# Kernel optimization log

Hardware: AMD Instinct MI355X
Metric: run time of the kernel (lower is better)

Reference implementation:

```python
import jax, jax.numpy as jnp
import numpy as np

D_MODEL = 1024
H = 16
D_K = D_MODEL // H
D_FF = 4096
EPS = 1e-6
NEG = -1e9


def setup_inputs() -> dict:
    key = jax.random.key(0)
    ks = jax.random.split(key, 8)
    B, S = 2, 2048
    src = jax.random.normal(ks[0], (B, S, D_MODEL), dtype=jnp.float32)
    src_mask = jnp.ones((B, 1, 1, S), dtype=jnp.int32)
    sc = 1.0 / np.sqrt(D_MODEL)
    wq = jax.random.normal(ks[1], (D_MODEL, D_MODEL), jnp.float32) * sc
    wk = jax.random.normal(ks[2], (D_MODEL, D_MODEL), jnp.float32) * sc
    wv = jax.random.normal(ks[3], (D_MODEL, D_MODEL), jnp.float32) * sc
    wo = jax.random.normal(ks[4], (D_MODEL, D_MODEL), jnp.float32) * sc
    w1 = jax.random.normal(ks[5], (D_FF, D_MODEL), jnp.float32) * sc
    b1 = jnp.zeros((D_FF,), jnp.float32)
    w2 = jax.random.normal(ks[6], (D_MODEL, D_FF), jnp.float32) * (1.0 / np.sqrt(D_FF))
    b2 = jnp.zeros((D_MODEL,), jnp.float32)
    a1 = jnp.ones((1,), jnp.float32)
    be1 = jnp.zeros((1,), jnp.float32)
    a2 = jnp.ones((1,), jnp.float32)
    be2 = jnp.zeros((1,), jnp.float32)
    return dict(src=src, src_mask=src_mask, wq=wq, wk=wk, wv=wv, wo=wo,
                w1=w1, b1=b1, w2=w2, b2=b2, a1=a1, be1=be1, a2=a2, be2=be2)


def layer_norm(x, alpha, bias):
    # torch: mean + unbiased std (ddof=1), eps added to std
    mean = jnp.mean(x, axis=-1, keepdims=True)
    std = jnp.sqrt(jnp.var(x, axis=-1, keepdims=True, ddof=1))
    return alpha * (x - mean) / (std + EPS) + bias


def mha(x, mask, wq, wk, wv, wo):
    B, S, _ = x.shape
    def split(t):  # [B,S,D] -> [B,H,S,D_K]
        return t.reshape(B, S, H, D_K).transpose(0, 2, 1, 3)
    q = split(x @ wq.T)
    k = split(x @ wk.T)
    v = split(x @ wv.T)
    scores = jnp.einsum('bhqd,bhkd->bhqk', q, k) / np.sqrt(D_K)
    scores = jnp.where(mask == 0, NEG, scores)
    attn = jax.nn.softmax(scores, axis=-1)
    out = jnp.einsum('bhqk,bhkd->bhqd', attn, v)
    out = out.transpose(0, 2, 1, 3).reshape(B, S, D_MODEL)
    return out @ wo.T


def reference(src, src_mask, wq, wk, wv, wo, w1, b1, w2, b2, a1, be1, a2, be2):
    x = layer_norm(src, a1, be1)
    src = src + mha(x, src_mask, wq, wk, wv, wo)
    x = layer_norm(src, a2, be2)
    ff = jax.nn.relu(x @ w1.T + b1) @ w2.T + b2
    return src + ff
```

## Files before the change

### kernel.cpp

```cpp
#include <hip/hip_runtime.h>
#include <hip/hip_bf16.h>

typedef unsigned short u16;
typedef unsigned int u32;
typedef float floatx4 __attribute__((ext_vector_type(4)));
typedef __bf16 bf16x8 __attribute__((ext_vector_type(8)));
typedef u16 ushort4v __attribute__((ext_vector_type(4)));
typedef u16 ushort8v __attribute__((ext_vector_type(8)));

#define DEVI static __device__ __forceinline__

DEVI u16 f2bf(float f) {
    u32 u = __builtin_bit_cast(u32, f);
    u += 0x7fffu + ((u >> 16) & 1u);
    return (u16)(u >> 16);
}
DEVI float bf2f(u16 h) { return __builtin_bit_cast(float, (u32)h << 16); }

DEVI float fexp2(float x) { return __builtin_amdgcn_exp2f(x); }

DEVI void async_cp16(const u16* g, u16* l) {
    __builtin_amdgcn_global_load_lds((const __attribute__((address_space(1))) u32*)g,
                                     (__attribute__((address_space(3))) u32*)l, 16, 0, 0);
}

template<int BM, int BN, int RW, int CW, bool QKV3, int NSPLIT, bool XSWZ,
         bool BIAS, bool RELU, bool RESID, bool OBF16>
__global__ __launch_bounds__(256) void gemm_nt(
    const u16* __restrict__ A,
    const u16* __restrict__ W0, const u16* __restrict__ W1, const u16* __restrict__ W2,
    const float* __restrict__ bias, const float* __restrict__ resid,
    void* __restrict__ o0, void* __restrict__ o1, void* __restrict__ o2,
    void* __restrict__ o3, int K, int lda, int Nper, int NX)
{
    static_assert(RW * CW == 4, "4 waves");
    constexpr int WM = BM / RW, WN = BN / CW;
    constexpr int MI = WM / 16, NI = WN / 16;
    __shared__ __align__(16) u16 As[2][BM * 32];
    __shared__ __align__(16) u16 Bs[2][BN * 32];
    const int tid = threadIdx.x;
    const int w = tid >> 6, lane = tid & 63;
    const int q = lane >> 4, ml = lane & 15;
    const int wr = w / CW, wc = w % CW;
    int bx = blockIdx.x, by = blockIdx.y;
    if (XSWZ) {
        const int gx = gridDim.x, gy = gridDim.y;
        int L = by * gx + bx;
        int xcd = L & 7, s = L >> 3;
        int mb = gy >> 3;
        by = xcd * mb + s % mb;
        bx = s / mb;
    }
    const int m0 = by * BM;
    size_t kbase = 0;
    const u16* W = W0;
    void* outp = o0;
    if (NSPLIT > 1) {
        int part = bx / NX; bx -= part * NX; kbase = (size_t)part * K;
        outp = (part == 0) ? o0 : (part == 1 ? o1 : (part == 2 ? o2 : o3));
    }
    int n0 = bx * BN;
    if (QKV3) {
        int sel = n0 / Nper;
        n0 -= sel * Nper;
        W = (sel == 0) ? W0 : (sel == 1 ? W1 : W2);
        outp = (sel == 0) ? o0 : (sel == 1 ? o1 : o2);
    }

    auto stage = [&](int buf, int kt) {
#pragma unroll
        for (int p = 0; p < BM / 64; ++p) {
            int g = p * 256 + tid;
            int r = g >> 2, s = g & 3;
            int c = s ^ ((r >> 1) & 3);
            async_cp16(A + (size_t)(m0 + r) * lda + kbase + kt + c * 8,
                       &As[buf][(p * 256 + w * 64) * 8]);
        }
#pragma unroll
        for (int p = 0; p < BN / 64; ++p) {
            int g = p * 256 + tid;
            int r = g >> 2, s = g & 3;
            int c = s ^ ((r >> 1) & 3);
            async_cp16(W + (size_t)(n0 + r) * lda + kbase + kt + c * 8,
                       &Bs[buf][(p * 256 + w * 64) * 8]);
        }
    };

    const floatx4 fzero = {0.f, 0.f, 0.f, 0.f};
    floatx4 acc[MI][NI];
#pragma unroll
    for (int i = 0; i < MI; ++i)
#pragma unroll
        for (int j = 0; j < NI; ++j) acc[i][j] = fzero;

    stage(0, 0);
    for (int it = 0, kt = 0; kt < K; ++it, kt += 32) {
        __syncthreads();
        if (kt + 32 < K) stage((it + 1) & 1, kt + 32);
        const u16* Asb = As[it & 1];
        const u16* Bsb = Bs[it & 1];
        bf16x8 af[MI], bfr[NI];
#pragma unroll
        for (int i = 0; i < MI; ++i) {
            int rm = wr * WM + i * 16 + ml;
            int s = q ^ ((rm >> 1) & 3);
            af[i] = *(const bf16x8*)&Asb[(rm * 4 + s) * 8];
        }
#pragma unroll
        for (int j = 0; j < NI; ++j) {
            int rn = wc * WN + j * 16 + ml;
            int s = q ^ ((rn >> 1) & 3);
            bfr[j] = *(const bf16x8*)&Bsb[(rn * 4 + s) * 8];
        }
#pragma unroll
        for (int i = 0; i < MI; ++i)
#pragma unroll
            for (int j = 0; j < NI; ++j)
                acc[i][j] = __builtin_amdgcn_mfma_f32_16x16x32_bf16(af[i], bfr[j], acc[i][j], 0, 0, 0);
    }

#pragma unroll
    for (int j = 0; j < NI; ++j) {
        int gn = n0 + wc * WN + j * 16 + ml;
        float bj = 0.f;
        if (BIAS) bj = bias[gn];
#pragma unroll
        for (int i = 0; i < MI; ++i) {
            int gm0 = m0 + wr * WM + i * 16 + q * 4;
#pragma unroll
            for (int r = 0; r < 4; ++r) {
                size_t idx = (size_t)(gm0 + r) * Nper + gn;
                float v = acc[i][j][r] + bj;
                if (RELU) v = fmaxf(v, 0.f);
                if (RESID) v += resid[idx];
                if (OBF16) ((u16*)outp)[idx] = f2bf(v);
                else       ((float*)outp)[idx] = v;
            }
        }
    }
}

__global__ __launch_bounds__(256, 4) void flash8(
    const u16* __restrict__ Q, const u16* __restrict__ Kg,
    const u16* __restrict__ Vt, const float* __restrict__ biasv,
    u16* __restrict__ O)
{
    __shared__ __align__(16) u16 Ks[2][2][32 * 64];
    __shared__ __align__(16) u16 Vs[2][2][64 * 32];
    const int tid = threadIdx.x;
    const int w = tid >> 6, lane = tid & 63;
    const int qw = w & 1, kv = w >> 1;
    const int q = lane >> 4, ml = lane & 15;
    const int b = blockIdx.y >> 4, h = blockIdx.y & 15;
    const size_t rowQ = (size_t)(b * 2048 + blockIdx.x * 64);
    const float KSC = 0.125f * 1.4426950408889634f;
    const floatx4 fzero = {0.f, 0.f, 0.f, 0.f};

    bf16x8 qa[2][2];
#pragma unroll
    for (int qg = 0; qg < 2; ++qg)
#pragma unroll
        for (int c = 0; c < 2; ++c)
            qa[qg][c] = *(const bf16x8*)&Q[(rowQ + qw * 32 + qg * 16 + ml) * 1024
                                           + h * 64 + q * 8 + c * 32];

    auto stage = [&](int buf, int it) {
        {
            int row = tid >> 3, sl = tid & 7;
            int ch = sl ^ ((row & 3) | (((row >> 3) & 1) << 2));
#pragma unroll
            for (int hf = 0; hf < 2; ++hf) {
                int s0 = hf * 1024 + it * 32;
                async_cp16(Kg + (size_t)(b * 2048 + s0 + row) * 1024 + h * 64 + ch * 8,
                           &Ks[hf][buf][(w * 64) * 8]);
            }
        }
        {
            int row = tid >> 2, sl = tid & 3;
            int ch = sl ^ ((row >> 1) & 3);
#pragma unroll
            for (int hf = 0; hf < 2; ++hf) {
                int s0 = hf * 1024 + it * 32;
                async_cp16(Vt + (size_t)(b * 1024 + h * 64 + row) * 2048 + s0 + ch * 8,
                           &Vs[hf][buf][(w * 64) * 8]);
            }
        }
    };

    floatx4 oacc[2][4];
    float lsum[2] = {0.f, 0.f};
#pragma unroll
    for (int qg = 0; qg < 2; ++qg)
#pragma unroll
        for (int d = 0; d < 4; ++d) oacc[qg][d] = fzero;

    const int swk = (ml & 3) | (((ml >> 2) & 1) << 2);
    const int re = ((ml >> 2) << 3) + (ml & 3);

    stage(0, 0);
    for (int it = 0; it < 32; ++it) {
        __syncthreads();
        if (it + 1 < 32) stage((it + 1) & 1, it + 1);
        const u16* Kb = Ks[kv][it & 1];
        const u16* Vb = Vs[kv][it & 1];
        const int s0 = kv * 1024 + it * 32;

        bf16x8 ke0 = *(const bf16x8*)&Kb[(re + 0) * 64 + ((0 + q) ^ swk) * 8];
        bf16x8 ke1 = *(const bf16x8*)&Kb[(re + 0) * 64 + ((4 + q) ^ swk) * 8];
        bf16x8 ko0 = *(const bf16x8*)&Kb[(re + 4) * 64 + ((0 + q) ^ swk) * 8];
        bf16x8 ko1 = *(const bf16x8*)&Kb[(re + 4) * 64 + ((4 + q) ^ swk) * 8];
        const float4 be = *(const float4*)&biasv[b * 2048 + s0 + q * 8];
        const float4 bo = *(const float4*)&biasv[b * 2048 + s0 + q * 8 + 4];
        bf16x8 pfrag[2];
#pragma unroll
        for (int qg = 0; qg < 2; ++qg) {
            floatx4 te = fzero, to = fzero;
            te = __builtin_amdgcn_mfma_f32_16x16x32_bf16(ke0, qa[qg][0], te, 0, 0, 0);
            te = __builtin_amdgcn_mfma_f32_16x16x32_bf16(ke1, qa[qg][1], te, 0, 0, 0);
            to = __builtin_amdgcn_mfma_f32_16x16x32_bf16(ko0, qa[qg][0], to, 0, 0, 0);
            to = __builtin_amdgcn_mfma_f32_16x16x32_bf16(ko1, qa[qg][1], to, 0, 0, 0);
            float pe0 = fexp2(fmaf(te[0], KSC, be.x));
            float pe1 = fexp2(fmaf(te[1], KSC, be.y));
            float pe2 = fexp2(fmaf(te[2], KSC, be.z));
            float pe3 = fexp2(fmaf(te[3], KSC, be.w));
            float po0 = fexp2(fmaf(to[0], KSC, bo.x));
            float po1 = fexp2(fmaf(to[1], KSC, bo.y));
            float po2 = fexp2(fmaf(to[2], KSC, bo.z));
            float po3 = fexp2(fmaf(to[3], KSC, bo.w));
            lsum[qg] += ((pe0 + pe1) + (pe2 + pe3)) + ((po0 + po1) + (po2 + po3));
            u32 pk[4];
            pk[0] = ((__builtin_bit_cast(u32, pe0) + 0x8000u) >> 16)
                  | ((__builtin_bit_cast(u32, pe1) + 0x8000u) & 0xffff0000u);
            pk[1] = ((__builtin_bit_cast(u32, pe2) + 0x8000u) >> 16)
                  | ((__builtin_bit_cast(u32, pe3) + 0x8000u) & 0xffff0000u);
            pk[2] = ((__builtin_bit_cast(u32, po0) + 0x8000u) >> 16)
                  | ((__builtin_bit_cast(u32, po1) + 0x8000u) & 0xffff0000u);
            pk[3] = ((__builtin_bit_cast(u32, po2) + 0x8000u) >> 16)
                  | ((__builtin_bit_cast(u32, po3) + 0x8000u) & 0xffff0000u);
            pfrag[qg] = __builtin_bit_cast(bf16x8, *(uint4*)pk);
        }
#pragma unroll
        for (int dt = 0; dt < 4; ++dt) {
            int vrow = dt * 16 + ml;
            bf16x8 vf = *(const bf16x8*)&Vb[vrow * 32 + ((q ^ ((vrow >> 1) & 3)) * 8)];
#pragma unroll
            for (int qg = 0; qg < 2; ++qg)
                oacc[qg][dt] = __builtin_amdgcn_mfma_f32_16x16x32_bf16(
                    vf, pfrag[qg], oacc[qg][dt], 0, 0, 0);
        }
    }

    __syncthreads();
    float* sO = (float*)&Ks[0][0][0];
    float* sL = (float*)&Vs[0][0][0];
    if (kv == 1) {
#pragma unroll
        for (int qg = 0; qg < 2; ++qg) {
            sL[(qw * 2 + qg) * 64 + lane] = lsum[qg];
#pragma unroll
            for (int dt = 0; dt < 4; ++dt)
                *(floatx4*)&sO[((qw * 2 + qg) * 4 + dt) * 256 + lane * 4] = oacc[qg][dt];
        }
    }
    __syncthreads();
    if (kv == 1) return;
#pragma unroll
    for (int qg = 0; qg < 2; ++qg) {
        lsum[qg] += sL[(qw * 2 + qg) * 64 + lane];
#pragma unroll
        for (int dt = 0; dt < 4; ++dt)
            oacc[qg][dt] += *(const floatx4*)&sO[((qw * 2 + qg) * 4 + dt) * 256 + lane * 4];
        float ls = lsum[qg];
        ls += __shfl_xor(ls, 16, 64);
        ls += __shfl_xor(ls, 32, 64);
        const float rcp = 1.f / ls;
        const size_t row = rowQ + qw * 32 + qg * 16 + ml;
#pragma unroll
        for (int dt = 0; dt < 4; ++dt)
#pragma unroll
            for (int rp = 0; rp < 4; rp += 2) {
                u32 pk = (u32)f2bf(oacc[qg][dt][rp] * rcp)
                       | ((u32)f2bf(oacc[qg][dt][rp + 1] * rcp) << 16);
                *(u32*)&O[row * 1024 + h * 64 + dt * 16 + q * 4 + rp] = pk;
            }
    }
}

__global__ __launch_bounds__(256) void vtrans(const u16* __restrict__ Vb, u16* __restrict__ Vt)
{
    __shared__ __align__(16) u16 T[64 * 72];
    const int tid = threadIdx.x;
    const int ct = blockIdx.x, rt = blockIdx.y;
    const int b = rt >> 5;
    const int s0 = (rt & 31) * 64;
    const int c0 = ct * 64;
#pragma unroll
    for (int p = 0; p < 2; ++p) {
        int slot = p * 256 + tid;
        int lr = slot >> 3, pc = slot & 7;
        bf16x8 v = *(const bf16x8*)&Vb[(size_t)(b * 2048 + s0 + lr) * 1024 + c0 + pc * 8];
        *(bf16x8*)&T[lr * 72 + pc * 8] = v;
    }
    __syncthreads();
#pragma unroll
    for (int p = 0; p < 2; ++p) {
        int slot = p * 256 + tid;
        int dc = slot >> 3, sc0 = (slot & 7) * 8;
        ushort8v o;
#pragma unroll
        for (int j = 0; j < 8; ++j) o[j] = T[(sc0 + j) * 72 + dc];
        *(ushort8v*)&Vt[(size_t)(b * 1024 + c0 + dc) * 2048 + s0 + sc0] = o;
    }
}

DEVI void ln_row(const float* __restrict__ x, float ga, float gb,
                 u16* __restrict__ y, int row, int tid)
{
    const float4 v = ((const float4*)(x + (size_t)row * 1024))[tid];
    float s = v.x + v.y + v.z + v.w;
    float ss = v.x * v.x + v.y * v.y + v.z * v.z + v.w * v.w;
#pragma unroll
    for (int d = 1; d < 64; d <<= 1) { s += __shfl_xor(s, d, 64); ss += __shfl_xor(ss, d, 64); }
    __shared__ float ps[4], pss[4];
    const int w = tid >> 6, lane = tid & 63;
    if (lane == 0) { ps[w] = s; pss[w] = ss; }
    __syncthreads();
    s = ps[0] + ps[1] + ps[2] + ps[3];
    ss = pss[0] + pss[1] + pss[2] + pss[3];
    float mean = s * (1.f / 1024.f);
    float var = fmaxf((ss - s * mean) * (1.f / 1023.f), 0.f);
    float sc = ga / (sqrtf(var) + 1e-6f);
    ushort4v o;
    o[0] = f2bf((v.x - mean) * sc + gb);
    o[1] = f2bf((v.y - mean) * sc + gb);
    o[2] = f2bf((v.z - mean) * sc + gb);
    o[3] = f2bf((v.w - mean) * sc + gb);
    ((ushort4v*)(y + (size_t)row * 1024))[tid] = o;
}

__global__ __launch_bounds__(256) void ln_bf16(const float* __restrict__ x,
    const float* __restrict__ ga, const float* __restrict__ gb, u16* __restrict__ y)
{
    ln_row(x, ga[0], gb[0], y, blockIdx.x, threadIdx.x);
}

__global__ __launch_bounds__(256) void prep(
    const float* __restrict__ wq, const float* __restrict__ wk,
    const float* __restrict__ wv, const float* __restrict__ wo,
    const float* __restrict__ w1, const float* __restrict__ w2,
    u16* __restrict__ wqb, u16* __restrict__ wkb, u16* __restrict__ wvb,
    u16* __restrict__ wob, u16* __restrict__ w1b, u16* __restrict__ w2b,
    const int* __restrict__ m, float* __restrict__ biasv,
    const float* __restrict__ src, const float* __restrict__ a1,
    const float* __restrict__ be1, u16* __restrict__ xln1)
{
    const int bx = blockIdx.x;
    if (bx < 12288) {
        size_t i = (size_t)bx * 256 + threadIdx.x;
        const float* s; u16* d; size_t off;
        if (i < 262144)       { s = wq; d = wqb; off = i; }
        else if (i < 524288)  { s = wk; d = wkb; off = i - 262144; }
        else if (i < 786432)  { s = wv; d = wvb; off = i - 524288; }
        else if (i < 1048576) { s = wo; d = wob; off = i - 786432; }
        else if (i < 2097152) { s = w1; d = w1b; off = i - 1048576; }
        else                  { s = w2; d = w2b; off = i - 2097152; }
        float4 v = ((const float4*)s)[off];
        ushort4v o = {f2bf(v.x), f2bf(v.y), f2bf(v.z), f2bf(v.w)};
        ((ushort4v*)d)[off] = o;
    } else if (bx < 12304) {
        int i = (bx - 12288) * 256 + threadIdx.x;
        biasv[i] = m[i] ? 0.f : -1.442695e9f;
    } else {
        ln_row(src, a1[0], be1[0], xln1, bx - 12304, threadIdx.x);
    }
}

__global__ __launch_bounds__(256) void ff2_fin(
    const u16* __restrict__ p0, const u16* __restrict__ p1,
    const float* __restrict__ b2, const float* __restrict__ resid,
    float* __restrict__ out)
{
    const size_t i = (size_t)blockIdx.x * 256 + threadIdx.x;
    ushort4v a = *(const ushort4v*)&p0[i * 4];
    ushort4v b = *(const ushort4v*)&p1[i * 4];
    float4 r = ((const float4*)resid)[i];
    float4 bb = ((const float4*)b2)[i & 255];
    float4 o;
    o.x = (bf2f(a[0]) + bf2f(b[0])) + r.x + bb.x;
    o.y = (bf2f(a[1]) + bf2f(b[1])) + r.y + bb.y;
    o.z = (bf2f(a[2]) + bf2f(b[2])) + r.z + bb.z;
    o.w = (bf2f(a[3]) + bf2f(b[3])) + r.w + bb.w;
    ((float4*)out)[i] = o;
}

extern "C" void kernel_launch(void* const* d_in, const int* in_sizes, int n_in,
                              void* d_out, int out_size, void* d_ws, size_t ws_size,
                              hipStream_t stream)
{
    const float* src = (const float*)d_in[0];
    const int* msk   = (const int*)d_in[1];
    const float* wq  = (const float*)d_in[2];
    const float* wk  = (const float*)d_in[3];
    const float* wv  = (const float*)d_in[4];
    const float* wo  = (const float*)d_in[5];
    const float* w1  = (const float*)d_in[6];
    const float* b1  = (const float*)d_in[7];
    const float* w2  = (const float*)d_in[8];
    const float* b2  = (const float*)d_in[9];
    const float* a1  = (const float*)d_in[10];
    const float* be1 = (const float*)d_in[11];
    const float* a2  = (const float*)d_in[12];
    const float* be2 = (const float*)d_in[13];
    float* out = (float*)d_out;

    char* ws = (char*)d_ws;
    const size_t MB = (size_t)1 << 20;
    u16* wqb  = (u16*)(ws + 0 * MB);
    u16* wkb  = (u16*)(ws + 2 * MB);
    u16* wvb  = (u16*)(ws + 4 * MB);
    u16* wob  = (u16*)(ws + 6 * MB);
    u16* w1b  = (u16*)(ws + 8 * MB);
    u16* w2b  = (u16*)(ws + 16 * MB);
    u16* xln1 = (u16*)(ws + 24 * MB);
    u16* attn = xln1;
    u16* Qb   = (u16*)(ws + 32 * MB);
    u16* xln2 = Qb;
    u16* Kb   = (u16*)(ws + 40 * MB);
    u16* Vb   = (u16*)(ws + 48 * MB);
    u16* Vt   = (u16*)(ws + 56 * MB);
    float* biasv = (float*)(ws + 64 * MB);
    u16* h1   = (u16*)(ws + 40 * MB);
    float* src2 = (float*)(ws + 72 * MB);
    u16* P0 = (u16*)(ws + 0 * MB);
    u16* P1 = (u16*)(ws + 24 * MB);

    prep<<<16400, 256, 0, stream>>>(wq, wk, wv, wo, w1, w2,
                                    wqb, wkb, wvb, wob, w1b, w2b,
                                    msk, biasv, src, a1, be1, xln1);

    gemm_nt<128, 128, 2, 2, true, 1, true, false, false, false, true><<<dim3(24, 32), 256, 0, stream>>>(
        xln1, wqb, wkb, wvb, nullptr, nullptr, Qb, Kb, Vb, nullptr, 1024, 1024, 1024, 0);

    vtrans<<<dim3(16, 64), 256, 0, stream>>>(Vb, Vt);

    flash8<<<dim3(32, 32), 256, 0, stream>>>(Qb, Kb, Vt, biasv, attn);

    gemm_nt<128, 64, 4, 1, false, 1, true, false, false, true, false><<<dim3(16, 32), 256, 0, stream>>>(
        attn, wob, nullptr, nullptr, nullptr, src, src2, nullptr, nullptr, nullptr,
        1024, 1024, 1024, 0);

    ln_bf16<<<4096, 256, 0, stream>>>(src2, a2, be2, xln2);

    gemm_nt<128, 128, 2, 2, false, 1, true, true, true, false, true><<<dim3(32, 32), 256, 0, stream>>>(
        xln2, w1b, nullptr, nullptr, b1, nullptr, h1, nullptr, nullptr, nullptr,
        1024, 1024, 4096, 0);

    gemm_nt<128, 128, 2, 2, false, 2, true, false, false, false, true><<<dim3(16, 32), 256, 0, stream>>>(
        h1, w2b, nullptr, nullptr, nullptr, nullptr, P0, P1, nullptr, nullptr,
        2048, 4096, 1024, 8);

    ff2_fin<<<4096, 256, 0, stream>>>(P0, P1, b2, src2, out);
}
```

Before: 357.8 us.

## Fuse V transpose into QKV GEMM epilogue and enlarge flash tile with triple buffering

The QKV GEMM now writes V directly in transposed layout from its epilogue, which removes the separate vtrans kernel and its round trip through memory. The attention kernel handles 128 query rows per block instead of 64, so each staged K/V tile is reused across twice as many queries. It also uses a three-deep LDS ring with explicit vmcnt waits and one barrier per iteration, and converts P to bf16 with a packed hardware instruction. The costs are higher register pressure (launch bounds lowered to 2), half as many attention blocks, and scattered 8-byte stores in the V epilogue.

```diff
diff --git a/kernel.cpp b/kernel.cpp
--- a/kernel.cpp
+++ b/kernel.cpp
@@ -19,13 +19,19 @@
 
 DEVI float fexp2(float x) { return __builtin_amdgcn_exp2f(x); }
 
+DEVI u32 cvtpk_bf16(float lo, float hi) {
+    u32 r;
+    asm("v_cvt_pk_bf16_f32 %0, %1, %2" : "=v"(r) : "v"(lo), "v"(hi));
+    return r;
+}
+
 DEVI void async_cp16(const u16* g, u16* l) {
     __builtin_amdgcn_global_load_lds((const __attribute__((address_space(1))) u32*)g,
                                      (__attribute__((address_space(3))) u32*)l, 16, 0, 0);
 }
 
 template<int BM, int BN, int RW, int CW, bool QKV3, int NSPLIT, bool XSWZ,
-         bool BIAS, bool RELU, bool RESID, bool OBF16>
+         bool BIAS, bool RELU, bool RESID, bool OBF16, bool VTW>
 __global__ __launch_bounds__(256) void gemm_nt(
     const u16* __restrict__ A,
     const u16* __restrict__ W0, const u16* __restrict__ W1, const u16* __restrict__ W2,
@@ -60,11 +66,13 @@
         outp = (part == 0) ? o0 : (part == 1 ? o1 : (part == 2 ? o2 : o3));
     }
     int n0 = bx * BN;
+    bool vwrite = false;
     if (QKV3) {
         int sel = n0 / Nper;
         n0 -= sel * Nper;
         W = (sel == 0) ? W0 : (sel == 1 ? W1 : W2);
         outp = (sel == 0) ? o0 : (sel == 1 ? o1 : o2);
+        if (VTW) vwrite = (sel == 2);
     }
 
     auto stage = [&](int buf, int kt) {
@@ -127,41 +135,47 @@
 #pragma unroll
         for (int i = 0; i < MI; ++i) {
             int gm0 = m0 + wr * WM + i * 16 + q * 4;
-#pragma unroll
-            for (int r = 0; r < 4; ++r) {
-                size_t idx = (size_t)(gm0 + r) * Nper + gn;
-                float v = acc[i][j][r] + bj;
-                if (RELU) v = fmaxf(v, 0.f);
-                if (RESID) v += resid[idx];
-                if (OBF16) ((u16*)outp)[idx] = f2bf(v);
-                else       ((float*)outp)[idx] = v;
+            if (VTW && vwrite) {
+                int bb = gm0 >> 11, sres = gm0 & 2047;
+                ushort4v o = {f2bf(acc[i][j][0]), f2bf(acc[i][j][1]),
+                              f2bf(acc[i][j][2]), f2bf(acc[i][j][3])};
+                *(ushort4v*)&((u16*)o3)[(size_t)(bb * 1024 + gn) * 2048 + sres] = o;
+            } else {
+#pragma unroll
+                for (int r = 0; r < 4; ++r) {
+                    size_t idx = (size_t)(gm0 + r) * Nper + gn;
+                    float v = acc[i][j][r] + bj;
+                    if (RELU) v = fmaxf(v, 0.f);
+                    if (RESID) v += resid[idx];
+                    if (OBF16) ((u16*)outp)[idx] = f2bf(v);
+                    else       ((float*)outp)[idx] = v;
+                }
             }
         }
     }
 }
 
-__global__ __launch_bounds__(256, 4) void flash8(
+__global__ __launch_bounds__(256, 2) void flash9(
     const u16* __restrict__ Q, const u16* __restrict__ Kg,
     const u16* __restrict__ Vt, const float* __restrict__ biasv,
     u16* __restrict__ O)
 {
-    __shared__ __align__(16) u16 Ks[2][2][32 * 64];
-    __shared__ __align__(16) u16 Vs[2][2][64 * 32];
+    __shared__ __align__(16) u16 smem[24576];
     const int tid = threadIdx.x;
     const int w = tid >> 6, lane = tid & 63;
     const int qw = w & 1, kv = w >> 1;
     const int q = lane >> 4, ml = lane & 15;
     const int b = blockIdx.y >> 4, h = blockIdx.y & 15;
-    const size_t rowQ = (size_t)(b * 2048 + blockIdx.x * 64);
+    const size_t rowQ = (size_t)(b * 2048 + blockIdx.x * 128);
     const float KSC = 0.125f * 1.4426950408889634f;
     const floatx4 fzero = {0.f, 0.f, 0.f, 0.f};
 
-    bf16x8 qa[2][2];
-#pragma unroll
-    for (int qg = 0; qg < 2; ++qg)
+    bf16x8 qa[4][2];
+#pragma unroll
+    for (int qg = 0; qg < 4; ++qg)
 #pragma unroll
         for (int c = 0; c < 2; ++c)
-            qa[qg][c] = *(const bf16x8*)&Q[(rowQ + qw * 32 + qg * 16 + ml) * 1024
+            qa[qg][c] = *(const bf16x8*)&Q[(rowQ + qw * 64 + qg * 16 + ml) * 1024
                                            + h * 64 + q * 8 + c * 32];
 
     auto stage = [&](int buf, int it) {
@@ -169,28 +183,26 @@
             int row = tid >> 3, sl = tid & 7;
             int ch = sl ^ ((row & 3) | (((row >> 3) & 1) << 2));
 #pragma unroll
-            for (int hf = 0; hf < 2; ++hf) {
-                int s0 = hf * 1024 + it * 32;
-                async_cp16(Kg + (size_t)(b * 2048 + s0 + row) * 1024 + h * 64 + ch * 8,
-                           &Ks[hf][buf][(w * 64) * 8]);
-            }
+            for (int hf = 0; hf < 2; ++hf)
+                async_cp16(Kg + (size_t)(b * 2048 + hf * 1024 + it * 32 + row) * 1024
+                               + h * 64 + ch * 8,
+                           &smem[(hf * 3 + buf) * 2048 + w * 512]);
         }
         {
             int row = tid >> 2, sl = tid & 3;
             int ch = sl ^ ((row >> 1) & 3);
 #pragma unroll
-            for (int hf = 0; hf < 2; ++hf) {
-                int s0 = hf * 1024 + it * 32;
-                async_cp16(Vt + (size_t)(b * 1024 + h * 64 + row) * 2048 + s0 + ch * 8,
-                           &Vs[hf][buf][(w * 64) * 8]);
-            }
+            for (int hf = 0; hf < 2; ++hf)
+                async_cp16(Vt + (size_t)(b * 1024 + h * 64 + row) * 2048
+                               + hf * 1024 + it * 32 + ch * 8,
+                           &smem[12288 + (hf * 3 + buf) * 2048 + w * 512]);
         }
     };
 
-    floatx4 oacc[2][4];
-    float lsum[2] = {0.f, 0.f};
-#pragma unroll
-    for (int qg = 0; qg < 2; ++qg)
+    floatx4 oacc[4][4];
+    float lsum[4] = {0.f, 0.f, 0.f, 0.f};
+#pragma unroll
+    for (int qg = 0; qg < 4; ++qg)
 #pragma unroll
         for (int d = 0; d < 4; ++d) oacc[qg][d] = fzero;
 
@@ -198,22 +210,28 @@
     const int re = ((ml >> 2) << 3) + (ml & 3);
 
     stage(0, 0);
+    stage(1, 1);
+    int cb = 0, nb = 2;
     for (int it = 0; it < 32; ++it) {
-        __syncthreads();
-        if (it + 1 < 32) stage((it + 1) & 1, it + 1);
-        const u16* Kb = Ks[kv][it & 1];
-        const u16* Vb = Vs[kv][it & 1];
+        asm volatile("s_waitcnt vmcnt(4)" ::: "memory");
+        __builtin_amdgcn_s_barrier();
+        __builtin_amdgcn_sched_barrier(0);
         const int s0 = kv * 1024 + it * 32;
+        const float4 be = *(const float4*)&biasv[b * 2048 + s0 + q * 8];
+        const float4 bo = *(const float4*)&biasv[b * 2048 + s0 + q * 8 + 4];
+        __builtin_amdgcn_sched_barrier(0);
+        stage(nb, it + 2 < 32 ? it + 2 : 31);
+
+        const u16* Kb = &smem[(kv * 3 + cb) * 2048];
+        const u16* Vb = &smem[12288 + (kv * 3 + cb) * 2048];
 
         bf16x8 ke0 = *(const bf16x8*)&Kb[(re + 0) * 64 + ((0 + q) ^ swk) * 8];
         bf16x8 ke1 = *(const bf16x8*)&Kb[(re + 0) * 64 + ((4 + q) ^ swk) * 8];
         bf16x8 ko0 = *(const bf16x8*)&Kb[(re + 4) * 64 + ((0 + q) ^ swk) * 8];
         bf16x8 ko1 = *(const bf16x8*)&Kb[(re + 4) * 64 + ((4 + q) ^ swk) * 8];
-        const float4 be = *(const float4*)&biasv[b * 2048 + s0 + q * 8];
-        const float4 bo = *(const float4*)&biasv[b * 2048 + s0 + q * 8 + 4];
-        bf16x8 pfrag[2];
-#pragma unroll
-        for (int qg = 0; qg < 2; ++qg) {
+        bf16x8 pfrag[4];
+#pragma unroll
+        for (int qg = 0; qg < 4; ++qg) {
             floatx4 te = fzero, to = fzero;
             te = __builtin_amdgcn_mfma_f32_16x16x32_bf16(ke0, qa[qg][0], te, 0, 0, 0);
             te = __builtin_amdgcn_mfma_f32_16x16x32_bf16(ke1, qa[qg][1], te, 0, 0, 0);
@@ -229,14 +247,10 @@
             float po3 = fexp2(fmaf(to[3], KSC, bo.w));
             lsum[qg] += ((pe0 + pe1) + (pe2 + pe3)) + ((po0 + po1) + (po2 + po3));
             u32 pk[4];
-            pk[0] = ((__builtin_bit_cast(u32, pe0) + 0x8000u) >> 16)
-                  | ((__builtin_bit_cast(u32, pe1) + 0x8000u) & 0xffff0000u);
-            pk[1] = ((__builtin_bit_cast(u32, pe2) + 0x8000u) >> 16)
-                  | ((__builtin_bit_cast(u32, pe3) + 0x8000u) & 0xffff0000u);
-            pk[2] = ((__builtin_bit_cast(u32, po0) + 0x8000u) >> 16)
-                  | ((__builtin_bit_cast(u32, po1) + 0x8000u) & 0xffff0000u);
-            pk[3] = ((__builtin_bit_cast(u32, po2) + 0x8000u) >> 16)
-                  | ((__builtin_bit_cast(u32, po3) + 0x8000u) & 0xffff0000u);
+            pk[0] = cvtpk_bf16(pe0, pe1);
+            pk[1] = cvtpk_bf16(pe2, pe3);
+            pk[2] = cvtpk_bf16(po0, po1);
+            pk[3] = cvtpk_bf16(po2, po3);
             pfrag[qg] = __builtin_bit_cast(bf16x8, *(uint4*)pk);
         }
 #pragma unroll
@@ -244,37 +258,39 @@
             int vrow = dt * 16 + ml;
             bf16x8 vf = *(const bf16x8*)&Vb[vrow * 32 + ((q ^ ((vrow >> 1) & 3)) * 8)];
 #pragma unroll
-            for (int qg = 0; qg < 2; ++qg)
+            for (int qg = 0; qg < 4; ++qg)
                 oacc[qg][dt] = __builtin_amdgcn_mfma_f32_16x16x32_bf16(
                     vf, pfrag[qg], oacc[qg][dt], 0, 0, 0);
         }
+        cb = cb == 2 ? 0 : cb + 1;
+        nb = nb == 2 ? 0 : nb + 1;
     }
 
     __syncthreads();
-    float* sO = (float*)&Ks[0][0][0];
-    float* sL = (float*)&Vs[0][0][0];
+    float* sO = (float*)smem;
+    float* sL = (float*)smem + 8192;
     if (kv == 1) {
 #pragma unroll
-        for (int qg = 0; qg < 2; ++qg) {
-            sL[(qw * 2 + qg) * 64 + lane] = lsum[qg];
+        for (int qg = 0; qg < 4; ++qg) {
+            sL[(qw * 4 + qg) * 64 + lane] = lsum[qg];
 #pragma unroll
             for (int dt = 0; dt < 4; ++dt)
-                *(floatx4*)&sO[((qw * 2 + qg) * 4 + dt) * 256 + lane * 4] = oacc[qg][dt];
+                *(floatx4*)&sO[((qw * 4 + qg) * 4 + dt) * 256 + lane * 4] = oacc[qg][dt];
         }
     }
     __syncthreads();
     if (kv == 1) return;
 #pragma unroll
-    for (int qg = 0; qg < 2; ++qg) {
-        lsum[qg] += sL[(qw * 2 + qg) * 64 + lane];
+    for (int qg = 0; qg < 4; ++qg) {
+        lsum[qg] += sL[(qw * 4 + qg) * 64 + lane];
 #pragma unroll
         for (int dt = 0; dt < 4; ++dt)
-            oacc[qg][dt] += *(const floatx4*)&sO[((qw * 2 + qg) * 4 + dt) * 256 + lane * 4];
+            oacc[qg][dt] += *(const floatx4*)&sO[((qw * 4 + qg) * 4 + dt) * 256 + lane * 4];
         float ls = lsum[qg];
         ls += __shfl_xor(ls, 16, 64);
         ls += __shfl_xor(ls, 32, 64);
         const float rcp = 1.f / ls;
-        const size_t row = rowQ + qw * 32 + qg * 16 + ml;
+        const size_t row = rowQ + qw * 64 + qg * 16 + ml;
 #pragma unroll
         for (int dt = 0; dt < 4; ++dt)
 #pragma unroll
@@ -283,33 +299,6 @@
                        | ((u32)f2bf(oacc[qg][dt][rp + 1] * rcp) << 16);
                 *(u32*)&O[row * 1024 + h * 64 + dt * 16 + q * 4 + rp] = pk;
             }
-    }
-}
-
-__global__ __launch_bounds__(256) void vtrans(const u16* __restrict__ Vb, u16* __restrict__ Vt)
-{
-    __shared__ __align__(16) u16 T[64 * 72];
-    const int tid = threadIdx.x;
-    const int ct = blockIdx.x, rt = blockIdx.y;
-    const int b = rt >> 5;
-    const int s0 = (rt & 31) * 64;
-    const int c0 = ct * 64;
-#pragma unroll
-    for (int p = 0; p < 2; ++p) {
-        int slot = p * 256 + tid;
-        int lr = slot >> 3, pc = slot & 7;
-        bf16x8 v = *(const bf16x8*)&Vb[(size_t)(b * 2048 + s0 + lr) * 1024 + c0 + pc * 8];
-        *(bf16x8*)&T[lr * 72 + pc * 8] = v;
-    }
-    __syncthreads();
-#pragma unroll
-    for (int p = 0; p < 2; ++p) {
-        int slot = p * 256 + tid;
-        int dc = slot >> 3, sc0 = (slot & 7) * 8;
-        ushort8v o;
-#pragma unroll
-        for (int j = 0; j < 8; ++j) o[j] = T[(sc0 + j) * 72 + dc];
-        *(ushort8v*)&Vt[(size_t)(b * 1024 + c0 + dc) * 2048 + s0 + sc0] = o;
     }
 }
 
@@ -426,7 +415,6 @@
     u16* Qb   = (u16*)(ws + 32 * MB);
     u16* xln2 = Qb;
     u16* Kb   = (u16*)(ws + 40 * MB);
-    u16* Vb   = (u16*)(ws + 48 * MB);
     u16* Vt   = (u16*)(ws + 56 * MB);
     float* biasv = (float*)(ws + 64 * MB);
     u16* h1   = (u16*)(ws + 40 * MB);
@@ -438,24 +426,22 @@
                                     wqb, wkb, wvb, wob, w1b, w2b,
                                     msk, biasv, src, a1, be1, xln1);
 
-    gemm_nt<128, 128, 2, 2, true, 1, true, false, false, false, true><<<dim3(24, 32), 256, 0, stream>>>(
-        xln1, wqb, wkb, wvb, nullptr, nullptr, Qb, Kb, Vb, nullptr, 1024, 1024, 1024, 0);
-
-    vtrans<<<dim3(16, 64), 256, 0, stream>>>(Vb, Vt);
-
-    flash8<<<dim3(32, 32), 256, 0, stream>>>(Qb, Kb, Vt, biasv, attn);
-
-    gemm_nt<128, 64, 4, 1, false, 1, true, false, false, true, false><<<dim3(16, 32), 256, 0, stream>>>(
+    gemm_nt<128, 128, 2, 2, true, 1, true, false, false, false, true, true><<<dim3(24, 32), 256, 0, stream>>>(
+        xln1, wqb, wkb, wvb, nullptr, nullptr, Qb, Kb, nullptr, Vt, 1024, 1024, 1024, 0);
+
+    flash9<<<dim3(16, 32), 256, 0, stream>>>(Qb, Kb, Vt, biasv, attn);
+
+    gemm_nt<128, 64, 4, 1, false, 1, true, false, false, true, false, false><<<dim3(16, 32), 256, 0, stream>>>(
         attn, wob, nullptr, nullptr, nullptr, src, src2, nullptr, nullptr, nullptr,
         1024, 1024, 1024, 0);
 
     ln_bf16<<<4096, 256, 0, stream>>>(src2, a2, be2, xln2);
 
-    gemm_nt<128, 128, 2, 2, false, 1, true, true, true, false, true><<<dim3(32, 32), 256, 0, stream>>>(
+    gemm_nt<128, 128, 2, 2, false, 1, true, true, true, false, true, false><<<dim3(32, 32), 256, 0, stream>>>(
         xln2, w1b, nullptr, nullptr, b1, nullptr, h1, nullptr, nullptr, nullptr,
         1024, 1024, 4096, 0);
 
-    gemm_nt<128, 128, 2, 2, false, 2, true, false, false, false, true><<<dim3(16, 32), 256, 0, stream>>>(
+    gemm_nt<128, 128, 2, 2, false, 2, true, false, false, false, true, false><<<dim3(16, 32), 256, 0, stream>>>(
         h1, w2b, nullptr, nullptr, nullptr, nullptr, P0, P1, nullptr, nullptr,
         2048, 4096, 1024, 8);
 
```

Measured after the change: 334.7 us. 1.07x faster.
